# Performance work log

Measured on AMD Instinct MI355X. Metric: run time of the kernel, lower is better.

## Reference

```python
import jax, jax.numpy as jnp
import numpy as np

B, S, E, H = 2, 2048, 1024, 16
HD = E // H


def setup_inputs() -> dict:
    key = jax.random.key(0)
    ks = jax.random.split(key, 9)
    s = 1.0 / np.sqrt(E)
    return {
        "x": jax.random.normal(ks[0], (B, S, E), dtype=jnp.float32),
        "wq": jax.random.uniform(ks[1], (E, E), jnp.float32, -s, s),
        "bq": jax.random.uniform(ks[2], (E,), jnp.float32, -s, s),
        "wk": jax.random.uniform(ks[3], (E, E), jnp.float32, -s, s),
        "bk": jax.random.uniform(ks[4], (E,), jnp.float32, -s, s),
        "wv": jax.random.uniform(ks[5], (E, E), jnp.float32, -s, s),
        "bv": jax.random.uniform(ks[6], (E,), jnp.float32, -s, s),
        "wo": jax.random.uniform(ks[7], (E, E), jnp.float32, -s, s),
        "bo": jax.random.uniform(ks[8], (E,), jnp.float32, -s, s),
    }


def reference(x, wq, bq, wk, bk, wv, bv, wo, bo):
    b, s, e = x.shape
    # QKV projections, reshape to [b, h, s, hd]
    def proj(w, bias):
        y = jnp.einsum('bse,ef->bsf', x, w.T) + bias
        return y.reshape(b, s, H, HD).transpose(0, 2, 1, 3)
    q = proj(wq, bq)
    k = proj(wk, bk)
    v = proj(wv, bv)
    score = jnp.einsum('bhqd,bhkd->bhqk', q, k) / jnp.sqrt(jnp.float32(HD))
    # original: exp(x)/sum(exp(x)) + 1e-8  == softmax(x) + 1e-8
    attn = jax.nn.softmax(score, axis=-1) + 1e-8
    out = jnp.einsum('bhqk,bhkd->bhqd', attn, v)
    out = out.transpose(0, 2, 1, 3).reshape(b, s, e)
    return jnp.einsum('bse,ef->bsf', out, wo.T) + bo
```

## Files before the change

### kernel.cpp

```cpp
#include <hip/hip_runtime.h>
#include <hip/hip_bf16.h>
#include <cstdint>

#define SS 2048
#define EE 1024
#define HH 16
#define HDD 64

typedef __attribute__((ext_vector_type(8))) __bf16 bf16x8;
typedef __attribute__((ext_vector_type(4))) float f32x4;

#define MFMA16(a, b, c) __builtin_amdgcn_mfma_f32_16x16x32_bf16((a), (b), (c), 0, 0, 0)

__device__ __forceinline__ unsigned short f2bf(float f) {
    unsigned int u = __builtin_bit_cast(unsigned int, f);
    u += 0x7FFFu + ((u >> 16) & 1u);
    return (unsigned short)(u >> 16);
}

__device__ __forceinline__ void gll16(const unsigned short* g, unsigned short* l) {
    __builtin_amdgcn_global_load_lds(
        (__attribute__((address_space(1))) unsigned int*)g,
        (__attribute__((address_space(3))) unsigned int*)l, 16, 0, 0);
}

__device__ __forceinline__ void pl32swap(unsigned int& a, unsigned int& b) {
#if __has_builtin(__builtin_amdgcn_permlane32_swap)
    auto r = __builtin_amdgcn_permlane32_swap(a, b, false, false);
    a = r[0]; b = r[1];
#else
    unsigned int as = __shfl_xor(a, 32, 64), bs = __shfl_xor(b, 32, 64);
    const bool hi = (threadIdx.x & 32) != 0;
    unsigned int na = hi ? bs : a, nb = hi ? b : as;
    a = na; b = nb;
#endif
}

__device__ __forceinline__ void pl16swap(unsigned int& a, unsigned int& b) {
#if __has_builtin(__builtin_amdgcn_permlane16_swap)
    auto r = __builtin_amdgcn_permlane16_swap(a, b, false, false);
    a = r[0]; b = r[1];
#else
    unsigned int as = __shfl_xor(a, 16, 64), bs = __shfl_xor(b, 16, 64);
    const bool odd = (threadIdx.x & 16) != 0;
    unsigned int na = odd ? bs : a, nb = odd ? b : as;
    a = na; b = nb;
#endif
}

__global__ __launch_bounds__(256) void cvt_all(
    const float* __restrict__ x, const float* __restrict__ wq, const float* __restrict__ wk,
    const float* __restrict__ wv, const float* __restrict__ wo,
    unsigned short* __restrict__ xb, unsigned short* __restrict__ wqb, unsigned short* __restrict__ wkb,
    unsigned short* __restrict__ wvb, unsigned short* __restrict__ wob) {
    int idx = blockIdx.x * 256 + threadIdx.x;
    int i4 = idx << 2;
    const float* src;
    unsigned short* dst;
    int off;
    if (i4 < 4194304) { src = x; dst = xb; off = i4; }
    else {
        int w = (i4 - 4194304) >> 20;
        off = (i4 - 4194304) & 1048575;
        if (w == 0) { src = wq; dst = wqb; }
        else if (w == 1) { src = wk; dst = wkb; }
        else if (w == 2) { src = wv; dst = wvb; }
        else { src = wo; dst = wob; }
    }
    float4 v = *(const float4*)&src[off];
    unsigned int p0 = (unsigned int)f2bf(v.x) | ((unsigned int)f2bf(v.y) << 16);
    unsigned int p1 = (unsigned int)f2bf(v.z) | ((unsigned int)f2bf(v.w) << 16);
    uint2 u; u.x = p0; u.y = p1;
    *(uint2*)&dst[off] = u;
}

template <int MODE, int BMT, int BNT>
__device__ __forceinline__ void gemm_core(
    unsigned short* __restrict__ lsA,
    unsigned short* __restrict__ lsB,
    const unsigned short* __restrict__ A, const unsigned short* __restrict__ W,
    const float* __restrict__ bias, void* __restrict__ out, int bm, int bn) {
    constexpr int IT = BMT / 32, JT = BNT / 32;
    constexpr int ASTR = BMT * 32, BSTR = BNT * 32;
    const int t = threadIdx.x;
    const int lane = t & 63, l15 = lane & 15, quad = lane >> 4;
    const int wave = t >> 6;
    const int wm = (wave >> 1) * (BMT / 2), wn = (wave & 1) * (BNT / 2);

    const int cg = ((t & 3) ^ ((t >> 3) & 3)) * 8;
    const unsigned short* ga = A + (size_t)(bm + (t >> 2)) * 1024 + cg;
    const unsigned short* gb = W + (size_t)(bn + (t >> 2)) * 1024 + cg;

    f32x4 acc[IT][JT];
    for (int i = 0; i < IT; i++)
        for (int j = 0; j < JT; j++) acc[i][j] = (f32x4){0.f, 0.f, 0.f, 0.f};

    const int swz = (l15 >> 1) & 3;

    gll16(ga, &lsA[t * 8]);
    if (BMT == 128) gll16(ga + 64 * 1024, &lsA[2048 + t * 8]);
    gll16(gb, &lsB[t * 8]);
    if (BNT == 128) gll16(gb + 64 * 1024, &lsB[2048 + t * 8]);

    for (int it = 0; it < 32; it++) {
        const int cur = it & 1, nxt = cur ^ 1;
        __syncthreads();

        if (it < 31) {
            const int k0 = (it + 1) * 32;
            gll16(ga + k0, &lsA[nxt * ASTR + t * 8]);
            if (BMT == 128) gll16(ga + k0 + 64 * 1024, &lsA[nxt * ASTR + 2048 + t * 8]);
            gll16(gb + k0, &lsB[nxt * BSTR + t * 8]);
            if (BNT == 128) gll16(gb + k0 + 64 * 1024, &lsB[nxt * BSTR + 2048 + t * 8]);
        }

        bf16x8 af[IT], bfr[JT];
        for (int i = 0; i < IT; i++)
            af[i] = *(const bf16x8*)&lsA[cur * ASTR + (wm + i * 16 + l15) * 32 + ((quad ^ swz) * 8)];
        for (int j = 0; j < JT; j++)
            bfr[j] = *(const bf16x8*)&lsB[cur * BSTR + (wn + j * 16 + l15) * 32 + ((quad ^ swz) * 8)];
        for (int i = 0; i < IT; i++)
            for (int j = 0; j < JT; j++) acc[i][j] = MFMA16(af[i], bfr[j], acc[i][j]);
    }

    for (int j = 0; j < JT; j++) {
        int n = bn + wn + j * 16 + l15;
        float bj = bias[n];
        for (int i = 0; i < IT; i++) {
            int m0 = bm + wm + i * 16 + quad * 4;
            int srow0 = m0 & 2047, bidx = m0 >> 11;
            if (MODE == 3) {
                size_t headb = ((size_t)bidx * HH + (n >> 6)) * (SS * HDD);
                size_t base = headb + (size_t)(srow0 >> 6) * 4096 +
                              (size_t)(((srow0 >> 4) & 3) * 8 + ((n & 63) >> 3)) * 128 + (n & 7);
                for (int rg = 0; rg < 4; rg++)
                    ((unsigned short*)out)[base + (size_t)((srow0 & 15) + rg) * 8] = f2bf(acc[i][j][rg] + bj);
            } else if (MODE == 4) {
                size_t headb = ((size_t)bidx * HH + (n >> 6)) * (SS * HDD);
                size_t addr = headb + (size_t)(srow0 >> 6) * 4096 + (size_t)((n & 63) >> 4) * 1024 +
                              (size_t)(((srow0 >> 5) & 1) * 4 + ((srow0 >> 3) & 3)) * 128 +
                              (size_t)(n & 15) * 8 + (srow0 & 7);
                float v0 = acc[i][j][0] + bj, v1 = acc[i][j][1] + bj;
                float v2 = acc[i][j][2] + bj, v3 = acc[i][j][3] + bj;
                uint2 w;
                w.x = (unsigned int)f2bf(v0) | ((unsigned int)f2bf(v1) << 16);
                w.y = (unsigned int)f2bf(v2) | ((unsigned int)f2bf(v3) << 16);
                *(uint2*)&((unsigned short*)out)[addr] = w;
            } else {
                for (int rg = 0; rg < 4; rg++) {
                    float val = acc[i][j][rg] + bj;
                    int m = m0 + rg;
                    if (MODE == 0) {
                        ((unsigned short*)out)[(((size_t)(m >> 11) * HH + (n >> 6)) * SS + (m & 2047)) * HDD + (n & 63)] = f2bf(val);
                    } else {
                        ((float*)out)[(size_t)m * 1024 + n] = val;
                    }
                }
            }
        }
    }
}

__global__ __launch_bounds__(256) void gemm_qkv(
    const unsigned short* __restrict__ xb,
    const unsigned short* __restrict__ wqb, const unsigned short* __restrict__ wkb,
    const unsigned short* __restrict__ wvb,
    const float* __restrict__ bq, const float* __restrict__ bk, const float* __restrict__ bv,
    unsigned short* qb, unsigned short* kb, unsigned short* vtb) {
    __shared__ unsigned short shA[2 * 4096];
    __shared__ unsigned short shB[2 * 4096];
    const int blk = blockIdx.x;
    const int u = blk & 7, r = blk >> 3;
    const int by = u + 8 * (r & 3);
    const int rest = r >> 2;
    const int bx = rest & 7, z = rest >> 3;
    if (z == 0)      gemm_core<0, 128, 128>(shA, shB, xb, wqb, bq, qb,  by * 128, bx * 128);
    else if (z == 1) gemm_core<3, 128, 128>(shA, shB, xb, wkb, bk, kb,  by * 128, bx * 128);
    else             gemm_core<4, 128, 128>(shA, shB, xb, wvb, bv, vtb, by * 128, bx * 128);
}

__global__ __launch_bounds__(256) void gemm_out(
    const unsigned short* __restrict__ ob, const unsigned short* __restrict__ wob,
    const float* __restrict__ bo, float* __restrict__ out) {
    __shared__ unsigned short shA[2 * 4096];
    __shared__ unsigned short shB[2 * 2048];
    const int blk = blockIdx.x;
    const int u = blk & 7, r = blk >> 3;
    const int by = u + 8 * (r & 3);
    const int bx = r >> 2;
    gemm_core<1, 128, 64>(shA, shB, ob, wob, bo, out, by * 128, bx * 64);
}

__global__ __launch_bounds__(512, 4) void attn_fwd(
    const unsigned short* __restrict__ qb, const unsigned short* __restrict__ kb,
    const unsigned short* __restrict__ vtb, unsigned short* __restrict__ ob) {
    __shared__ unsigned short sh[32768];
    unsigned short* lsK = sh;
    unsigned short* lsV = sh + 16384;
    const int t = threadIdx.x, lane = t & 63, l15 = lane & 15, quad = lane >> 4;
    const int wave = t >> 6;
    const int half = wave >> 2;
    const int wq = wave & 3;
    const int tg = t & 255;
    const int blk = blockIdx.x;
    const int u = blk & 7, r = blk >> 3;
    const int bh = u + 8 * (r & 3);
    const int qt = r >> 2;
    const size_t hoff = (size_t)bh * (SS * HDD);
    const float C = 0.125f * 1.44269504088896f;

    bf16x8 qf[2][2];
    const int qrow = qt * 128 + wq * 32;
    for (int i = 0; i < 2; i++)
        for (int ks = 0; ks < 2; ks++) {
            bf16x8 raw = *(const bf16x8*)&qb[hoff + (size_t)(qrow + i * 16 + l15) * HDD + ks * 32 + quad * 8];
            unsigned short tmp[8];
            *(bf16x8*)tmp = raw;
            for (int j = 0; j < 8; j++) {
                float f = __builtin_bit_cast(float, (unsigned int)tmp[j] << 16);
                tmp[j] = f2bf(f * C);
            }
            qf[i][ks] = *(const bf16x8*)tmp;
        }

    unsigned short onesbuf[8];
    for (int j = 0; j < 8; j++) onesbuf[j] = 0x3F80;
    const bf16x8 onesf = *(const bf16x8*)onesbuf;

    f32x4 lacc[2];
    f32x4 o[2][4];
    for (int i = 0; i < 2; i++) {
        lacc[i] = (f32x4){0.f, 0.f, 0.f, 0.f};
        for (int jh = 0; jh < 4; jh++) o[i][jh] = (f32x4){0.f, 0.f, 0.f, 0.f};
    }

    const unsigned short* gk = kb + hoff + (size_t)half * 16 * 4096;
    const unsigned short* gv = vtb + hoff + (size_t)half * 16 * 4096;
    const int foff = quad * 128 + l15 * 8;

    auto stage = [&](int buf, int tile) {
        unsigned short* dk = lsK + buf * 8192 + half * 4096;
        unsigned short* dv = lsV + buf * 8192 + half * 4096;
        const unsigned short* sk = gk + tile * 4096;
        const unsigned short* sv = gv + tile * 4096;
        gll16(sk + tg * 8, dk + tg * 8);
        gll16(sk + 2048 + tg * 8, dk + 2048 + tg * 8);
        gll16(sv + tg * 8, dv + tg * 8);
        gll16(sv + 2048 + tg * 8, dv + 2048 + tg * 8);
    };

    bf16x8 pfp[2][2];
    bf16x8 vfp[4][2];

    auto qk_pack = [&](const unsigned short* myK) {
        bf16x8 kfr[4][2];
        for (int j = 0; j < 4; j++)
            for (int ks = 0; ks < 2; ks++)
                kfr[j][ks] = *(const bf16x8*)&myK[j * 1024 + ks * 512 + foff];
        f32x4 st[2][4];
        for (int j = 0; j < 4; j++)
            for (int i = 0; i < 2; i++) {
                f32x4 z = (f32x4){0.f, 0.f, 0.f, 0.f};
                z = MFMA16(kfr[j][0], qf[i][0], z);
                z = MFMA16(kfr[j][1], qf[i][1], z);
                st[i][j] = z;
            }
        for (int i = 0; i < 2; i++) {
            unsigned int W[4][2];
            for (int j = 0; j < 4; j++) {
                float e0 = __builtin_amdgcn_exp2f(st[i][j][0]);
                float e1 = __builtin_amdgcn_exp2f(st[i][j][1]);
                float e2 = __builtin_amdgcn_exp2f(st[i][j][2]);
                float e3 = __builtin_amdgcn_exp2f(st[i][j][3]);
                W[j][0] = (__builtin_bit_cast(unsigned int, e0) >> 16) |
                          (__builtin_bit_cast(unsigned int, e1) & 0xFFFF0000u);
                W[j][1] = (__builtin_bit_cast(unsigned int, e2) >> 16) |
                          (__builtin_bit_cast(unsigned int, e3) & 0xFFFF0000u);
            }
            unsigned int P0[4], P1[4];
            for (int h = 0; h < 2; h++) {
                unsigned int x = W[0][h], y = W[1][h];
                pl32swap(x, y);
                pl16swap(x, y);
                P0[h] = x; P0[2 + h] = y;
                unsigned int x2 = W[2][h], y2 = W[3][h];
                pl32swap(x2, y2);
                pl16swap(x2, y2);
                P1[h] = x2; P1[2 + h] = y2;
            }
            union { unsigned int u4[4]; bf16x8 v; } cv0, cv1;
            for (int p = 0; p < 4; p++) { cv0.u4[p] = P0[p]; cv1.u4[p] = P1[p]; }
            pfp[i][0] = cv0.v;
            pfp[i][1] = cv1.v;
        }
    };
    auto readV = [&](const unsigned short* myV) {
        for (int jh = 0; jh < 4; jh++) {
            vfp[jh][0] = *(const bf16x8*)&myV[jh * 1024 + foff];
            vfp[jh][1] = *(const bf16x8*)&myV[jh * 1024 + 512 + foff];
        }
    };
    auto pv = [&]() {
        __builtin_amdgcn_s_setprio(1);
        for (int jh = 0; jh < 4; jh++)
            for (int i = 0; i < 2; i++) {
                o[i][jh] = MFMA16(pfp[i][0], vfp[jh][0], o[i][jh]);
                o[i][jh] = MFMA16(pfp[i][1], vfp[jh][1], o[i][jh]);
            }
        for (int i = 0; i < 2; i++) {
            lacc[i] = MFMA16(pfp[i][0], onesf, lacc[i]);
            lacc[i] = MFMA16(pfp[i][1], onesf, lacc[i]);
        }
        __builtin_amdgcn_s_setprio(0);
    };

    stage(0, 0);

    __syncthreads();
    stage(1, 1);
    qk_pack(lsK + half * 4096);
    readV(lsV + half * 4096);

    for (int kt = 1; kt < 16; kt++) {
        const int cur = kt & 1;
        __syncthreads();
        if (kt < 15) stage(cur ^ 1, kt + 1);
        pv();
        const unsigned short* myK = lsK + cur * 8192 + half * 4096;
        const unsigned short* myV = lsV + cur * 8192 + half * 4096;
        qk_pack(myK);
        readV(myV);
    }
    pv();

    __syncthreads();
    float* cb = (float*)sh;
    float* lb = cb + 8192;
    const int lslot = wq * 64 + lane;
    if (half == 1) {
        for (int i = 0; i < 2; i++)
            for (int jh = 0; jh < 4; jh++)
                for (int rg = 0; rg < 4; rg++)
                    cb[(i * 16 + jh * 4 + rg) * 256 + lslot] = o[i][jh][rg];
        for (int i = 0; i < 2; i++)
            for (int rg = 0; rg < 4; rg++)
                lb[(i * 4 + rg) * 256 + lslot] = lacc[i][rg];
    }
    __syncthreads();
    if (half == 0) {
        const int b = bh >> 4, h = bh & 15;
        for (int i = 0; i < 2; i++)
            for (int rg = 0; rg < 4; rg++) {
                float inv = 1.f / (lacc[i][rg] + lb[(i * 4 + rg) * 256 + lslot]);
                int srow = qrow + i * 16 + quad * 4 + rg;
                size_t rowoff = ((size_t)b * SS + srow) * EE + h * 64;
                for (int jh = 0; jh < 4; jh++) {
                    float val = o[i][jh][rg] + cb[(i * 16 + jh * 4 + rg) * 256 + lslot];
                    ob[rowoff + jh * 16 + l15] = f2bf(val * inv);
                }
            }
    }
}

extern "C" void kernel_launch(void* const* d_in, const int* in_sizes, int n_in,
                              void* d_out, int out_size, void* d_ws, size_t ws_size,
                              hipStream_t stream) {
    const float* x  = (const float*)d_in[0];
    const float* wq = (const float*)d_in[1];
    const float* bq = (const float*)d_in[2];
    const float* wk = (const float*)d_in[3];
    const float* bk = (const float*)d_in[4];
    const float* wv = (const float*)d_in[5];
    const float* bv = (const float*)d_in[6];
    const float* wo = (const float*)d_in[7];
    const float* bo = (const float*)d_in[8];

    char* ws = (char*)d_ws;
    unsigned short* xb  = (unsigned short*)(ws + 0);
    unsigned short* wqb = (unsigned short*)(ws + 8388608);
    unsigned short* wkb = (unsigned short*)(ws + 10485760);
    unsigned short* wvb = (unsigned short*)(ws + 12582912);
    unsigned short* wob = (unsigned short*)(ws + 14680064);
    unsigned short* qb  = (unsigned short*)(ws + 16777216);
    unsigned short* kb  = (unsigned short*)(ws + 25165824);
    unsigned short* vtb = (unsigned short*)(ws + 33554432);
    unsigned short* ob  = xb;

    cvt_all<<<8192, 256, 0, stream>>>(x, wq, wk, wv, wo, xb, wqb, wkb, wvb, wob);
    gemm_qkv<<<768, 256, 0, stream>>>(xb, wqb, wkb, wvb, bq, bk, bv, qb, kb, vtb);
    attn_fwd<<<512, 512, 0, stream>>>(qb, kb, vtb, ob);
    gemm_out<<<512, 256, 0, stream>>>(ob, wob, bo, (float*)d_out);
}
```

Measured before the change: 187.9 us.

## Rewrite QKV GEMM as dedicated 256x256 tile kernel with K=64 double buffering

```diff
diff --git a/kernel.cpp b/kernel.cpp
--- a/kernel.cpp
+++ b/kernel.cpp
@@ -128,55 +128,13 @@
         float bj = bias[n];
         for (int i = 0; i < IT; i++) {
             int m0 = bm + wm + i * 16 + quad * 4;
-            int srow0 = m0 & 2047, bidx = m0 >> 11;
-            if (MODE == 3) {
-                size_t headb = ((size_t)bidx * HH + (n >> 6)) * (SS * HDD);
-                size_t base = headb + (size_t)(srow0 >> 6) * 4096 +
-                              (size_t)(((srow0 >> 4) & 3) * 8 + ((n & 63) >> 3)) * 128 + (n & 7);
-                for (int rg = 0; rg < 4; rg++)
-                    ((unsigned short*)out)[base + (size_t)((srow0 & 15) + rg) * 8] = f2bf(acc[i][j][rg] + bj);
-            } else if (MODE == 4) {
-                size_t headb = ((size_t)bidx * HH + (n >> 6)) * (SS * HDD);
-                size_t addr = headb + (size_t)(srow0 >> 6) * 4096 + (size_t)((n & 63) >> 4) * 1024 +
-                              (size_t)(((srow0 >> 5) & 1) * 4 + ((srow0 >> 3) & 3)) * 128 +
-                              (size_t)(n & 15) * 8 + (srow0 & 7);
-                float v0 = acc[i][j][0] + bj, v1 = acc[i][j][1] + bj;
-                float v2 = acc[i][j][2] + bj, v3 = acc[i][j][3] + bj;
-                uint2 w;
-                w.x = (unsigned int)f2bf(v0) | ((unsigned int)f2bf(v1) << 16);
-                w.y = (unsigned int)f2bf(v2) | ((unsigned int)f2bf(v3) << 16);
-                *(uint2*)&((unsigned short*)out)[addr] = w;
-            } else {
-                for (int rg = 0; rg < 4; rg++) {
-                    float val = acc[i][j][rg] + bj;
-                    int m = m0 + rg;
-                    if (MODE == 0) {
-                        ((unsigned short*)out)[(((size_t)(m >> 11) * HH + (n >> 6)) * SS + (m & 2047)) * HDD + (n & 63)] = f2bf(val);
-                    } else {
-                        ((float*)out)[(size_t)m * 1024 + n] = val;
-                    }
-                }
-            }
-        }
-    }
-}
-
-__global__ __launch_bounds__(256) void gemm_qkv(
-    const unsigned short* __restrict__ xb,
-    const unsigned short* __restrict__ wqb, const unsigned short* __restrict__ wkb,
-    const unsigned short* __restrict__ wvb,
-    const float* __restrict__ bq, const float* __restrict__ bk, const float* __restrict__ bv,
-    unsigned short* qb, unsigned short* kb, unsigned short* vtb) {
-    __shared__ unsigned short shA[2 * 4096];
-    __shared__ unsigned short shB[2 * 4096];
-    const int blk = blockIdx.x;
-    const int u = blk & 7, r = blk >> 3;
-    const int by = u + 8 * (r & 3);
-    const int rest = r >> 2;
-    const int bx = rest & 7, z = rest >> 3;
-    if (z == 0)      gemm_core<0, 128, 128>(shA, shB, xb, wqb, bq, qb,  by * 128, bx * 128);
-    else if (z == 1) gemm_core<3, 128, 128>(shA, shB, xb, wkb, bk, kb,  by * 128, bx * 128);
-    else             gemm_core<4, 128, 128>(shA, shB, xb, wvb, bv, vtb, by * 128, bx * 128);
+            for (int rg = 0; rg < 4; rg++) {
+                float val = acc[i][j][rg] + bj;
+                int m = m0 + rg;
+                ((float*)out)[(size_t)m * 1024 + n] = val;
+            }
+        }
+    }
 }
 
 __global__ __launch_bounds__(256) void gemm_out(
@@ -189,6 +147,144 @@
     const int by = u + 8 * (r & 3);
     const int bx = r >> 2;
     gemm_core<1, 128, 64>(shA, shB, ob, wob, bo, out, by * 128, bx * 64);
+}
+
+__global__ __launch_bounds__(512, 2) void gemm_qkv(
+    const unsigned short* __restrict__ xb,
+    const unsigned short* __restrict__ wqb, const unsigned short* __restrict__ wkb,
+    const unsigned short* __restrict__ wvb,
+    const float* __restrict__ bq, const float* __restrict__ bk, const float* __restrict__ bv,
+    unsigned short* qb, unsigned short* kb, unsigned short* vtb) {
+    __shared__ unsigned short sh[65536];
+    unsigned short* lsA = sh;
+    unsigned short* lsB = sh + 32768;
+
+    const int blk = blockIdx.x;
+    const int z = blk >> 6;
+    const int rem = blk & 63;
+    const int bm = (rem & 15) * 256;
+    const int bn = (rem >> 4) * 256;
+
+    const unsigned short* W;
+    const float* bias;
+    unsigned short* outp;
+    if (z == 0)      { W = wqb; bias = bq; outp = qb; }
+    else if (z == 1) { W = wkb; bias = bk; outp = kb; }
+    else             { W = wvb; bias = bv; outp = vtb; }
+
+    const int t = threadIdx.x;
+    const int lane = t & 63, l15 = lane & 15, quad = lane >> 4;
+    const int wave = t >> 6;
+    const int wm_ = (wave >> 2) * 128;
+    const int wn_ = (wave & 3) * 64;
+
+    const int trow = t >> 3, tcol = t & 7;
+    const int scol = ((tcol ^ (trow & 7)) << 3);
+    const unsigned short* ga = xb + (size_t)(bm + trow) * 1024 + scol;
+    const unsigned short* gb = W + (size_t)(bn + trow) * 1024 + scol;
+
+    f32x4 acc[8][4];
+    for (int mi = 0; mi < 8; mi++)
+        for (int nj = 0; nj < 4; nj++) acc[mi][nj] = (f32x4){0.f, 0.f, 0.f, 0.f};
+
+    const int sw = l15 & 7;
+    const int aRowBase = wm_ + l15;
+    const int bRowBase = wn_ + l15;
+
+    auto stageA = [&](int buf, int kt) {
+        const unsigned short* s = ga + kt * 64;
+        unsigned short* d = lsA + buf * 16384 + t * 8;
+        gll16(s, d);
+        gll16(s + 65536, d + 4096);
+        gll16(s + 131072, d + 8192);
+        gll16(s + 196608, d + 12288);
+    };
+    auto stageB = [&](int buf, int kt) {
+        const unsigned short* s = gb + kt * 64;
+        unsigned short* d = lsB + buf * 16384 + t * 8;
+        gll16(s, d);
+        gll16(s + 65536, d + 4096);
+        gll16(s + 131072, d + 8192);
+        gll16(s + 196608, d + 12288);
+    };
+
+    stageA(0, 0);
+    stageB(0, 0);
+
+    for (int kt = 0; kt < 16; kt++) {
+        const int cur = kt & 1, nxt = cur ^ 1;
+
+        if (kt < 15) {
+            stageA(nxt, kt + 1);
+            asm volatile("s_waitcnt vmcnt(4)" ::: "memory");
+        } else {
+            asm volatile("s_waitcnt vmcnt(0)" ::: "memory");
+        }
+        __builtin_amdgcn_s_barrier();
+        __builtin_amdgcn_sched_barrier(0);
+
+        const unsigned short* curA = lsA + cur * 16384;
+        const unsigned short* curB = lsB + cur * 16384;
+
+        bf16x8 afr[8], bfr[4];
+        for (int mi = 0; mi < 8; mi++)
+            afr[mi] = *(const bf16x8*)&curA[(aRowBase + mi * 16) * 64 + ((quad ^ sw) << 3)];
+        for (int nj = 0; nj < 4; nj++)
+            bfr[nj] = *(const bf16x8*)&curB[(bRowBase + nj * 16) * 64 + ((quad ^ sw) << 3)];
+        __builtin_amdgcn_s_setprio(1);
+        for (int mi = 0; mi < 8; mi++)
+            for (int nj = 0; nj < 4; nj++)
+                acc[mi][nj] = MFMA16(afr[mi], bfr[nj], acc[mi][nj]);
+        __builtin_amdgcn_s_setprio(0);
+
+        if (kt < 15) stageB(nxt, kt + 1);
+
+        for (int mi = 0; mi < 8; mi++)
+            afr[mi] = *(const bf16x8*)&curA[(aRowBase + mi * 16) * 64 + (((4 + quad) ^ sw) << 3)];
+        for (int nj = 0; nj < 4; nj++)
+            bfr[nj] = *(const bf16x8*)&curB[(bRowBase + nj * 16) * 64 + (((4 + quad) ^ sw) << 3)];
+        __builtin_amdgcn_s_setprio(1);
+        for (int mi = 0; mi < 8; mi++)
+            for (int nj = 0; nj < 4; nj++)
+                acc[mi][nj] = MFMA16(afr[mi], bfr[nj], acc[mi][nj]);
+        __builtin_amdgcn_s_setprio(0);
+
+        __builtin_amdgcn_s_barrier();
+        __builtin_amdgcn_sched_barrier(0);
+    }
+
+    for (int nj = 0; nj < 4; nj++) {
+        int n = bn + wn_ + nj * 16 + l15;
+        float bj = bias[n];
+        for (int mi = 0; mi < 8; mi++) {
+            int m0 = bm + wm_ + mi * 16 + quad * 4;
+            int srow0 = m0 & 2047, bidx = m0 >> 11;
+            if (z == 0) {
+                for (int rg = 0; rg < 4; rg++) {
+                    int m = m0 + rg;
+                    outp[(((size_t)(m >> 11) * HH + (n >> 6)) * SS + (m & 2047)) * HDD + (n & 63)] =
+                        f2bf(acc[mi][nj][rg] + bj);
+                }
+            } else if (z == 1) {
+                size_t headb = ((size_t)bidx * HH + (n >> 6)) * (SS * HDD);
+                size_t base = headb + (size_t)(srow0 >> 6) * 4096 +
+                              (size_t)(((srow0 >> 4) & 3) * 8 + ((n & 63) >> 3)) * 128 + (n & 7);
+                for (int rg = 0; rg < 4; rg++)
+                    outp[base + (size_t)((srow0 & 15) + rg) * 8] = f2bf(acc[mi][nj][rg] + bj);
+            } else {
+                size_t headb = ((size_t)bidx * HH + (n >> 6)) * (SS * HDD);
+                size_t addr = headb + (size_t)(srow0 >> 6) * 4096 + (size_t)((n & 63) >> 4) * 1024 +
+                              (size_t)(((srow0 >> 5) & 1) * 4 + ((srow0 >> 3) & 3)) * 128 +
+                              (size_t)(n & 15) * 8 + (srow0 & 7);
+                float v0 = acc[mi][nj][0] + bj, v1 = acc[mi][nj][1] + bj;
+                float v2 = acc[mi][nj][2] + bj, v3 = acc[mi][nj][3] + bj;
+                uint2 w;
+                w.x = (unsigned int)f2bf(v0) | ((unsigned int)f2bf(v1) << 16);
+                w.y = (unsigned int)f2bf(v2) | ((unsigned int)f2bf(v3) << 16);
+                *(uint2*)&outp[addr] = w;
+            }
+        }
+    }
 }
 
 __global__ __launch_bounds__(512, 4) void attn_fwd(
@@ -387,7 +483,7 @@
     unsigned short* ob  = xb;
 
     cvt_all<<<8192, 256, 0, stream>>>(x, wq, wk, wv, wo, xb, wqb, wkb, wvb, wob);
-    gemm_qkv<<<768, 256, 0, stream>>>(xb, wqb, wkb, wvb, bq, bk, bv, qb, kb, vtb);
+    gemm_qkv<<<192, 512, 0, stream>>>(xb, wqb, wkb, wvb, bq, bk, bv, qb, kb, vtb);
     attn_fwd<<<512, 512, 0, stream>>>(qb, kb, vtb, ob);
     gemm_out<<<512, 256, 0, stream>>>(ob, wob, bo, (float*)d_out);
 }
```

Measured after the change: 217.3 us. +15.6%, slower.
